# Kernel optimization log

Hardware: AMD Instinct MI355X
Metric: run time of the kernel (lower is better)

The kernel has to match this reference:

```python
import math
import jax, jax.numpy as jnp
import numpy as np

L = 2          # num_layers
B = 2          # micro batch
S = 2048       # seq_length
H = 1024       # hidden_size
NH = 16        # num_attention_heads
DH = 64        # kv_channels (head dim)
FF = 4096      # ffn_hidden_size
EPS = 1e-5
STD = 0.0048


def setup_inputs() -> dict:
    key = jax.random.key(0)
    ks = jax.random.split(key, 12)
    out_std = STD / math.sqrt(2.0 * L)
    # ALiBi slopes for NH=16 (power of 2)
    start = 2.0 ** (-2.0 ** (-(math.log2(NH) - 3)))
    slopes = np.array([start * start ** i for i in range(NH)], dtype=np.float32)
    alibi = slopes[None, :, None, None] * np.arange(S, dtype=np.float32)[None, None, None, :]
    alibi = jnp.asarray(np.broadcast_to(alibi, (B, NH, 1, S)))  # [B, NH, 1, S]
    return {
        "hidden_states": jax.random.normal(ks[0], (B, S, H), jnp.float32),
        "alibi": alibi,
        "qkv_w": jax.random.normal(ks[1], (L, 3 * NH * DH, H), jnp.float32) * STD,
        "qkv_b": jnp.zeros((L, 3 * NH * DH), jnp.float32),
        "dense_w": jax.random.normal(ks[2], (L, H, NH * DH), jnp.float32) * out_std,
        "dense_b": jnp.zeros((L, H), jnp.float32),
        "mlp_w1": jax.random.normal(ks[3], (L, FF, H), jnp.float32) * STD,
        "mlp_b1": jnp.zeros((L, FF), jnp.float32),
        "mlp_w2": jax.random.normal(ks[4], (L, H, FF), jnp.float32) * out_std,
        "mlp_b2": jnp.zeros((L, H), jnp.float32),
        "ln1_w": jnp.ones((L, H), jnp.float32),
        "ln1_b": jnp.zeros((L, H), jnp.float32),
        "ln2_w": jnp.ones((L, H), jnp.float32),
        "ln2_b": jnp.zeros((L, H), jnp.float32),
    }


def _layernorm(x, w, b):
    mu = jnp.mean(x, axis=-1, keepdims=True)
    var = jnp.mean(jnp.square(x - mu), axis=-1, keepdims=True)
    return (x - mu) * jax.lax.rsqrt(var + EPS) * w + b


def _layer(x, alibi, causal, layer_number, qkv_w, qkv_b, dense_w, dense_b,
           mlp_w1, mlp_b1, mlp_w2, mlp_b2, ln1_w, ln1_b, ln2_w, ln2_b):
    # --- attention ---
    h = _layernorm(x, ln1_w, ln1_b)
    qkv = h @ qkv_w.T + qkv_b                       # [B, S, 3*NH*DH]
    q, k, v = jnp.split(qkv, 3, axis=-1)
    q = q.reshape(B, S, NH, DH).transpose(0, 2, 1, 3)  # [B, NH, S, DH]
    k = k.reshape(B, S, NH, DH).transpose(0, 2, 1, 3)
    v = v.reshape(B, S, NH, DH).transpose(0, 2, 1, 3)
    norm_factor = math.sqrt(DH) * layer_number
    beta = 1.0 / layer_number
    alpha = 1.0 / norm_factor
    scores = beta * alibi + alpha * jnp.einsum("bhqd,bhkd->bhqk", q, k)
    # ScaleMaskSoftmax: scale by layer_number, causal mask fill -10000, softmax
    scores = scores * layer_number
    scores = jnp.where(causal, scores, jnp.float32(-10000.0))
    probs = jax.nn.softmax(scores, axis=-1)
    ctx = jnp.einsum("bhqk,bhkd->bhqd", probs, v)   # [B, NH, S, DH]
    ctx = ctx.transpose(0, 2, 1, 3).reshape(B, S, NH * DH)
    attn_out = ctx @ dense_w.T + dense_b
    x = x + attn_out
    # --- MLP ---
    h2 = _layernorm(x, ln2_w, ln2_b)
    m = jax.nn.gelu(h2 @ mlp_w1.T + mlp_b1, approximate=False)
    m = m @ mlp_w2.T + mlp_b2
    return x + m


def reference(hidden_states, alibi, qkv_w, qkv_b, dense_w, dense_b,
              mlp_w1, mlp_b1, mlp_w2, mlp_b2, ln1_w, ln1_b, ln2_w, ln2_b):
    causal = jnp.tril(jnp.ones((S, S), dtype=bool))[None, None]  # [1,1,S,S]
    x = hidden_states
    for l in range(L):
        x = _layer(x, alibi, causal, l + 1,
                   qkv_w[l], qkv_b[l], dense_w[l], dense_b[l],
                   mlp_w1[l], mlp_b1[l], mlp_w2[l], mlp_b2[l],
                   ln1_w[l], ln1_b[l], ln2_w[l], ln2_b[l])
    return x
```

## Files before the change

kernel.cpp:

```cpp
#include <hip/hip_runtime.h>
#include <cstdint>
#include <cmath>

#define SS 2048
#define HH 1024

typedef __bf16 bf16_t;
typedef __bf16 bf16x8 __attribute__((ext_vector_type(8)));
typedef __bf16 bf16x4 __attribute__((ext_vector_type(4)));
typedef float  f32x4  __attribute__((ext_vector_type(4)));

union U32P { unsigned u; bf16_t h[2]; };

__device__ __forceinline__ void async_load16(const void* g, void* l) {
  __builtin_amdgcn_global_load_lds(
      (__attribute__((address_space(1))) void*)(g),
      (__attribute__((address_space(3))) void*)(l), 16, 0, 0);
}

__global__ __launch_bounds__(256) void cvt_kernel(const float* __restrict__ in,
                                                  bf16_t* __restrict__ out) {
  size_t i = (size_t)blockIdx.x * 256 + threadIdx.x;
  f32x4 v = ((const f32x4*)in)[i];
  bf16x4 o;
  o[0] = (bf16_t)v[0]; o[1] = (bf16_t)v[1]; o[2] = (bf16_t)v[2]; o[3] = (bf16_t)v[3];
  ((bf16x4*)out)[i] = o;
}

__global__ __launch_bounds__(256) void ln_kernel(const float* __restrict__ x,
                                                 const float* __restrict__ w,
                                                 const float* __restrict__ b,
                                                 bf16_t* __restrict__ out) {
  const int row = blockIdx.x;
  const int tid = threadIdx.x;
  const f32x4 v = ((const f32x4*)(x + (size_t)row * HH))[tid];
  float s  = v[0] + v[1] + v[2] + v[3];
  float s2 = v[0]*v[0] + v[1]*v[1] + v[2]*v[2] + v[3]*v[3];
#pragma unroll
  for (int o = 1; o < 64; o <<= 1) { s += __shfl_xor(s, o); s2 += __shfl_xor(s2, o); }
  __shared__ float r1[4], r2[4];
  if ((tid & 63) == 0) { r1[tid >> 6] = s; r2[tid >> 6] = s2; }
  __syncthreads();
  float ts  = r1[0] + r1[1] + r1[2] + r1[3];
  float ts2 = r2[0] + r2[1] + r2[2] + r2[3];
  float mu  = ts * (1.0f / HH);
  float var = ts2 * (1.0f / HH) - mu * mu;
  float rstd = rsqrtf(var + 1e-5f);
  f32x4 wv = ((const f32x4*)w)[tid];
  f32x4 bv = ((const f32x4*)b)[tid];
  bf16x4 o;
#pragma unroll
  for (int j = 0; j < 4; ++j) o[j] = (bf16_t)((v[j] - mu) * rstd * wv[j] + bv[j]);
  ((bf16x4*)(out + (size_t)row * HH))[tid] = o;
}

__device__ __forceinline__ float gelu_f(float x) {
  return 0.5f * x * (1.0f + erff(x * 0.70710678118654752f));
}

__global__ __launch_bounds__(256) void fuse_add(float* __restrict__ x,
                                                const bf16_t* __restrict__ p0,
                                                const bf16_t* __restrict__ p1,
                                                const float* __restrict__ bias) {
  size_t i = (size_t)blockIdx.x * 256 + threadIdx.x;
  f32x4 xv = ((f32x4*)x)[i];
  bf16x4 a = ((const bf16x4*)p0)[i];
  bf16x4 b4 = ((const bf16x4*)p1)[i];
  f32x4 bv = ((const f32x4*)bias)[i & 255];
#pragma unroll
  for (int j = 0; j < 4; ++j) xv[j] += (float)a[j] + (float)b4[j] + bv[j];
  ((f32x4*)x)[i] = xv;
}

template <int EPI>
__global__ __launch_bounds__(256) void gemm_bt(const bf16_t* __restrict__ A,
                                               const bf16_t* __restrict__ W,
                                               const float* __restrict__ bias,
                                               bf16_t* __restrict__ outb,
                                               int M, int N, int K) {
  __shared__ __align__(16) bf16_t As[128 * 64];
  __shared__ __align__(16) bf16_t Bs[128 * 64];
  const int tid = threadIdx.x;
  const int w = tid >> 6, lane = tid & 63;
  const int m16 = lane & 15, quad = lane >> 4;
  const int wm = w & 1, wn = w >> 1;
  const int n0 = blockIdx.x * 128, m0 = blockIdx.y * 128;

  f32x4 acc[4][4];
#pragma unroll
  for (int i = 0; i < 4; ++i)
#pragma unroll
    for (int j = 0; j < 4; ++j) acc[i][j] = (f32x4){0.f, 0.f, 0.f, 0.f};

  int rowi[4], gci[4];
#pragma unroll
  for (int i = 0; i < 4; ++i) {
    int p = (w * 4 + i) * 64 + lane;
    rowi[i] = p >> 3;
    gci[i] = ((lane & 7) ^ (rowi[i] & 7)) * 8;
  }

  for (int kt = 0; kt < K; kt += 64) {
    __syncthreads();
#pragma unroll
    for (int i = 0; i < 4; ++i) {
      async_load16(A + (size_t)(m0 + rowi[i]) * K + kt + gci[i], &As[(w * 4 + i) * 512]);
      async_load16(W + (size_t)(n0 + rowi[i]) * K + kt + gci[i], &Bs[(w * 4 + i) * 512]);
    }
    __syncthreads();
#pragma unroll
    for (int kk = 0; kk < 2; ++kk) {
      bf16x8 af[4], bfv[4];
#pragma unroll
      for (int mi = 0; mi < 4; ++mi) {
        int row = wm * 64 + mi * 16 + m16;
        int cpos = (kk * 4 + quad) ^ (row & 7);
        af[mi] = *(const bf16x8*)&As[row * 64 + cpos * 8];
      }
#pragma unroll
      for (int ni = 0; ni < 4; ++ni) {
        int row = wn * 64 + ni * 16 + m16;
        int cpos = (kk * 4 + quad) ^ (row & 7);
        bfv[ni] = *(const bf16x8*)&Bs[row * 64 + cpos * 8];
      }
#pragma unroll
      for (int mi = 0; mi < 4; ++mi)
#pragma unroll
        for (int ni = 0; ni < 4; ++ni)
          acc[mi][ni] = __builtin_amdgcn_mfma_f32_16x16x32_bf16(af[mi], bfv[ni],
                                                                acc[mi][ni], 0, 0, 0);
    }
  }

#pragma unroll
  for (int ni = 0; ni < 4; ++ni) {
    int col = n0 + wn * 64 + ni * 16 + m16;
    float bv = bias[col];
#pragma unroll
    for (int mi = 0; mi < 4; ++mi) {
      int rowb = m0 + wm * 64 + mi * 16 + quad * 4;
#pragma unroll
      for (int r = 0; r < 4; ++r) {
        size_t idx = (size_t)(rowb + r) * N + col;
        float v = acc[mi][ni][r] + bv;
        if constexpr (EPI == 1) v = gelu_f(v);
        outb[idx] = (bf16_t)v;
      }
    }
  }
}

__global__ __launch_bounds__(256) void gemm_sk2(const bf16_t* __restrict__ A,
                                                const bf16_t* __restrict__ W,
                                                bf16_t* __restrict__ p0,
                                                bf16_t* __restrict__ p1,
                                                int M, int N, int K) {
  __shared__ __align__(16) bf16_t As[128 * 64];
  __shared__ __align__(16) bf16_t Bs[128 * 64];
  const int tid = threadIdx.x;
  const int w = tid >> 6, lane = tid & 63;
  const int m16 = lane & 15, quad = lane >> 4;
  const int wm = w & 1, wn = w >> 1;
  const int n0 = blockIdx.x * 128, m0 = blockIdx.y * 128;
  const int z = blockIdx.z;
  const int kbeg = z * (K >> 1), kend = kbeg + (K >> 1);
  bf16_t* outb = z ? p1 : p0;

  f32x4 acc[4][4];
#pragma unroll
  for (int i = 0; i < 4; ++i)
#pragma unroll
    for (int j = 0; j < 4; ++j) acc[i][j] = (f32x4){0.f, 0.f, 0.f, 0.f};

  int rowi[4], gci[4];
#pragma unroll
  for (int i = 0; i < 4; ++i) {
    int p = (w * 4 + i) * 64 + lane;
    rowi[i] = p >> 3;
    gci[i] = ((lane & 7) ^ (rowi[i] & 7)) * 8;
  }

  for (int kt = kbeg; kt < kend; kt += 64) {
    __syncthreads();
#pragma unroll
    for (int i = 0; i < 4; ++i) {
      async_load16(A + (size_t)(m0 + rowi[i]) * K + kt + gci[i], &As[(w * 4 + i) * 512]);
      async_load16(W + (size_t)(n0 + rowi[i]) * K + kt + gci[i], &Bs[(w * 4 + i) * 512]);
    }
    __syncthreads();
#pragma unroll
    for (int kk = 0; kk < 2; ++kk) {
      bf16x8 af[4], bfv[4];
#pragma unroll
      for (int mi = 0; mi < 4; ++mi) {
        int row = wm * 64 + mi * 16 + m16;
        int cpos = (kk * 4 + quad) ^ (row & 7);
        af[mi] = *(const bf16x8*)&As[row * 64 + cpos * 8];
      }
#pragma unroll
      for (int ni = 0; ni < 4; ++ni) {
        int row = wn * 64 + ni * 16 + m16;
        int cpos = (kk * 4 + quad) ^ (row & 7);
        bfv[ni] = *(const bf16x8*)&Bs[row * 64 + cpos * 8];
      }
#pragma unroll
      for (int mi = 0; mi < 4; ++mi)
#pragma unroll
        for (int ni = 0; ni < 4; ++ni)
          acc[mi][ni] = __builtin_amdgcn_mfma_f32_16x16x32_bf16(af[mi], bfv[ni],
                                                                acc[mi][ni], 0, 0, 0);
    }
  }

#pragma unroll
  for (int ni = 0; ni < 4; ++ni) {
    int col = n0 + wn * 64 + ni * 16 + m16;
#pragma unroll
    for (int mi = 0; mi < 4; ++mi) {
      int rowb = m0 + wm * 64 + mi * 16 + quad * 4;
#pragma unroll
      for (int r = 0; r < 4; ++r) {
        size_t idx = (size_t)(rowb + r) * N + col;
        outb[idx] = (bf16_t)acc[mi][ni][r];
      }
    }
  }
}

__global__ __launch_bounds__(256) void attn_kernel(const bf16_t* __restrict__ qkv,
                                                   bf16_t* __restrict__ ctx) {
  const int qt = 31 - blockIdx.y;
  const int bh = blockIdx.x;
  const int b = bh >> 4, h = bh & 15;
  const int tid = threadIdx.x;
  const int w = tid >> 6, lane = tid & 63;
  const int m16 = lane & 15, quad = lane >> 4;

  __shared__ __align__(16) bf16_t Vt[2][64 * 72];
  __shared__ __align__(16) bf16_t Pl[4][16 * 72];

  const float slope2 = __builtin_amdgcn_exp2f(-0.70710678118654752f * (float)(h + 1))
                       * 1.4426950408889634f;
  const int wt = (int)((30.0f / slope2 + 63.0f) * 0.015625f);
  const int kt0 = (qt - wt > 0) ? (qt - wt) : 0;

  const int q_abs = qt * 64 + w * 16 + m16;
  float alkb[16];
#pragma unroll
  for (int kn = 0; kn < 4; ++kn)
#pragma unroll
    for (int r = 0; r < 4; ++r)
      alkb[kn * 4 + r] = slope2 * (float)(kt0 * 64 + kn * 16 + quad * 4 + r - q_abs);
  const float d64 = slope2 * 64.0f;

  const int qrow = qt * 64 + w * 16 + m16;
  const bf16_t* qbase = qkv + (size_t)(b * SS + qrow) * 3072 + h * 64;
  const bf16x8 bq0 = *(const bf16x8*)(qbase + quad * 8);
  const bf16x8 bq1 = *(const bf16x8*)(qbase + 32 + quad * 8);

  const bf16_t* kbase = qkv + (size_t)(b * SS + m16) * 3072 + 1024 + h * 64 + quad * 8;
  const int kp2 = (tid & 31) * 2, vd0 = (tid >> 5) * 8;
  const bf16_t* vsrc = qkv + (size_t)(b * SS + kp2) * 3072 + 2048 + h * 64 + vd0;
  const int ql = w * 16 + m16;
  constexpr float C = 0.18033688011112042f;

  f32x4 acc[4];
#pragma unroll
  for (int i = 0; i < 4; ++i) acc[i] = (f32x4){0.f, 0.f, 0.f, 0.f};
  float rs_l = 0.f;

  bf16x8 ak[4][2], v0, v1;
  {
    const bf16_t* kb = kbase + (size_t)kt0 * 64 * 3072;
#pragma unroll
    for (int kn = 0; kn < 4; ++kn) {
      ak[kn][0] = *(const bf16x8*)(kb + (size_t)(kn * 16) * 3072);
      ak[kn][1] = *(const bf16x8*)(kb + (size_t)(kn * 16) * 3072 + 32);
    }
    const bf16_t* vs = vsrc + (size_t)kt0 * 64 * 3072;
    v0 = *(const bf16x8*)(vs);
    v1 = *(const bf16x8*)(vs + 3072);
  }
#pragma unroll
  for (int j = 0; j < 8; ++j) {
    U32P pk; pk.h[0] = v0[j]; pk.h[1] = v1[j];
    *(unsigned*)&Vt[kt0 & 1][(vd0 + j) * 72 + kp2] = pk.u;
  }

  for (int kt = kt0; kt <= qt; ++kt) {
    __syncthreads();

    bf16x8 nk[4][2], nv0 = v0, nv1 = v1;
    if (kt < qt) {
      const bf16_t* kb = kbase + (size_t)(kt + 1) * 64 * 3072;
#pragma unroll
      for (int kn = 0; kn < 4; ++kn) {
        nk[kn][0] = *(const bf16x8*)(kb + (size_t)(kn * 16) * 3072);
        nk[kn][1] = *(const bf16x8*)(kb + (size_t)(kn * 16) * 3072 + 32);
      }
      const bf16_t* nsrc = vsrc + (size_t)(kt + 1) * 64 * 3072;
      nv0 = *(const bf16x8*)(nsrc);
      nv1 = *(const bf16x8*)(nsrc + 3072);
    } else {
#pragma unroll
      for (int kn = 0; kn < 4; ++kn) { nk[kn][0] = ak[kn][0]; nk[kn][1] = ak[kn][1]; }
    }

    float p[16];
    const bool diag = (kt == qt);
#pragma unroll
    for (int kn = 0; kn < 4; ++kn) {
      f32x4 z = (f32x4){0.f, 0.f, 0.f, 0.f};
      z = __builtin_amdgcn_mfma_f32_16x16x32_bf16(ak[kn][0], bq0, z, 0, 0, 0);
      z = __builtin_amdgcn_mfma_f32_16x16x32_bf16(ak[kn][1], bq1, z, 0, 0, 0);
#pragma unroll
      for (int r = 0; r < 4; ++r) {
        float s = fmaf(z[r], C, alkb[kn * 4 + r]);
        if (diag) {
          int kl = kn * 16 + quad * 4 + r;
          if (kl > ql) s = -INFINITY;
        }
        float e = __builtin_amdgcn_exp2f(s);
        p[kn * 4 + r] = e;
        rs_l += e;
      }
    }
#pragma unroll
    for (int i = 0; i < 16; ++i) alkb[i] += d64;

#pragma unroll
    for (int kn = 0; kn < 4; ++kn) {
      U32P a, c;
      a.h[0] = (bf16_t)p[kn * 4 + 0]; a.h[1] = (bf16_t)p[kn * 4 + 1];
      c.h[0] = (bf16_t)p[kn * 4 + 2]; c.h[1] = (bf16_t)p[kn * 4 + 3];
      uint2 pk; pk.x = a.u; pk.y = c.u;
      *(uint2*)&Pl[w][m16 * 72 + kn * 16 + quad * 4] = pk;
    }
    const bf16_t* vt = &Vt[kt & 1][0];
    bf16x8 bp0 = *(const bf16x8*)&Pl[w][m16 * 72 + quad * 8];
    bf16x8 bp1 = *(const bf16x8*)&Pl[w][m16 * 72 + 32 + quad * 8];
#pragma unroll
    for (int ni = 0; ni < 4; ++ni) {
      bf16x8 av0 = *(const bf16x8*)&vt[(ni * 16 + m16) * 72 + quad * 8];
      bf16x8 av1 = *(const bf16x8*)&vt[(ni * 16 + m16) * 72 + 32 + quad * 8];
      acc[ni] = __builtin_amdgcn_mfma_f32_16x16x32_bf16(av0, bp0, acc[ni], 0, 0, 0);
      acc[ni] = __builtin_amdgcn_mfma_f32_16x16x32_bf16(av1, bp1, acc[ni], 0, 0, 0);
    }

    if (kt < qt) {
#pragma unroll
      for (int j = 0; j < 8; ++j) {
        U32P pk; pk.h[0] = nv0[j]; pk.h[1] = nv1[j];
        *(unsigned*)&Vt[(kt + 1) & 1][(vd0 + j) * 72 + kp2] = pk.u;
      }
    }
#pragma unroll
    for (int kn = 0; kn < 4; ++kn) { ak[kn][0] = nk[kn][0]; ak[kn][1] = nk[kn][1]; }
    v0 = nv0; v1 = nv1;
  }

  rs_l += __shfl_xor(rs_l, 16);
  rs_l += __shfl_xor(rs_l, 32);
  const float inv_l = 1.0f / rs_l;
  bf16_t* cb = ctx + (size_t)(b * SS + qt * 64 + w * 16 + m16) * 1024 + h * 64;
#pragma unroll
  for (int ni = 0; ni < 4; ++ni) {
    U32P a, c;
    a.h[0] = (bf16_t)(acc[ni][0] * inv_l); a.h[1] = (bf16_t)(acc[ni][1] * inv_l);
    c.h[0] = (bf16_t)(acc[ni][2] * inv_l); c.h[1] = (bf16_t)(acc[ni][3] * inv_l);
    uint2 pk; pk.x = a.u; pk.y = c.u;
    *(uint2*)(cb + ni * 16 + quad * 4) = pk;
  }
}

extern "C" void kernel_launch(void* const* d_in, const int* in_sizes, int n_in,
                              void* d_out, int out_size, void* d_ws, size_t ws_size,
                              hipStream_t stream) {
  const float* hs    = (const float*)d_in[0];
  const float* qkvw  = (const float*)d_in[2];
  const float* qkvb  = (const float*)d_in[3];
  const float* dw    = (const float*)d_in[4];
  const float* db    = (const float*)d_in[5];
  const float* w1    = (const float*)d_in[6];
  const float* b1    = (const float*)d_in[7];
  const float* w2    = (const float*)d_in[8];
  const float* b2    = (const float*)d_in[9];
  const float* ln1w  = (const float*)d_in[10];
  const float* ln1b  = (const float*)d_in[11];
  const float* ln2w  = (const float*)d_in[12];
  const float* ln2b  = (const float*)d_in[13];
  float* x = (float*)d_out;

  char* ws = (char*)d_ws;
  bf16_t* wqc = (bf16_t*)(ws + 0);
  bf16_t* wdc = (bf16_t*)(ws + 12582912);
  bf16_t* w1c = (bf16_t*)(ws + 16777216);
  bf16_t* w2c = (bf16_t*)(ws + 33554432);
  bf16_t* hb  = (bf16_t*)(ws + 50331648);
  bf16_t* qm  = (bf16_t*)(ws + 58720256);
  bf16_t* cx  = (bf16_t*)(ws + 92274688);
  bf16_t* dp0 = qm;
  bf16_t* dp1 = qm + (size_t)4096 * 1024;

  hipMemcpyAsync(x, hs, (size_t)4096 * 1024 * 4, hipMemcpyDeviceToDevice, stream);
  cvt_kernel<<<6144, 256, 0, stream>>>(qkvw, wqc);
  cvt_kernel<<<2048, 256, 0, stream>>>(dw, wdc);
  cvt_kernel<<<8192, 256, 0, stream>>>(w1, w1c);
  cvt_kernel<<<8192, 256, 0, stream>>>(w2, w2c);

  for (int l = 0; l < 2; ++l) {
    ln_kernel<<<4096, 256, 0, stream>>>(x, ln1w + l * 1024, ln1b + l * 1024, hb);
    gemm_bt<0><<<dim3(24, 32), 256, 0, stream>>>(hb, wqc + (size_t)l * 3145728,
        qkvb + l * 3072, qm, 4096, 3072, 1024);
    attn_kernel<<<dim3(32, 32), 256, 0, stream>>>(qm, cx);
    gemm_sk2<<<dim3(8, 32, 2), 256, 0, stream>>>(cx, wdc + (size_t)l * 1048576,
        dp0, dp1, 4096, 1024, 1024);
    fuse_add<<<4096, 256, 0, stream>>>(x, dp0, dp1, db + l * 1024);
    ln_kernel<<<4096, 256, 0, stream>>>(x, ln2w + l * 1024, ln2b + l * 1024, hb);
    gemm_bt<1><<<dim3(32, 32), 256, 0, stream>>>(hb, w1c + (size_t)l * 4194304,
        b1 + l * 4096, qm, 4096, 4096, 1024);
    gemm_sk2<<<dim3(8, 32, 2), 256, 0, stream>>>(qm, w2c + (size_t)l * 4194304,
        hb, cx, 4096, 1024, 4096);
    fuse_add<<<4096, 256, 0, stream>>>(x, hb, cx, b2 + l * 1024);
  }
}
```

Before: 706.8 us.

## Emit per-head Q/K and transposed V from QKV GEMM; one-wave LDS-free attention

The QKV GEMM epilogue now writes Q row-major, K in a per-(batch, head) contiguous layout and V transposed per head. This lets the attention kernel load MFMA operands straight from global memory. Attention is rewritten so each wave independently handles 16 query rows, stepping 32 keys at a time with no shared memory or block barriers. The ALiBi slope constant now matches the reference slopes, which also changes the truncated key window. Weight conversion to bf16 moves into the per-layer loop to shrink the workspace. The trade-off is scattered, strided epilogue stores for K and V, and more global-load traffic per wave.

```diff
diff --git a/kernel.cpp b/kernel.cpp
--- a/kernel.cpp
+++ b/kernel.cpp
@@ -145,6 +145,99 @@
         float v = acc[mi][ni][r] + bv;
         if constexpr (EPI == 1) v = gelu_f(v);
         outb[idx] = (bf16_t)v;
+      }
+    }
+  }
+}
+
+__global__ __launch_bounds__(256) void gemm_qkv(const bf16_t* __restrict__ A,
+                                                const bf16_t* __restrict__ W,
+                                                const float* __restrict__ bias,
+                                                bf16_t* __restrict__ qq,
+                                                bf16_t* __restrict__ kpb,
+                                                bf16_t* __restrict__ vtb) {
+  __shared__ __align__(16) bf16_t As[128 * 64];
+  __shared__ __align__(16) bf16_t Bs[128 * 64];
+  const int K = 1024;
+  const int tid = threadIdx.x;
+  const int w = tid >> 6, lane = tid & 63;
+  const int m16 = lane & 15, quad = lane >> 4;
+  const int wm = w & 1, wn = w >> 1;
+  const int n0 = blockIdx.x * 128, m0 = blockIdx.y * 128;
+
+  f32x4 acc[4][4];
+#pragma unroll
+  for (int i = 0; i < 4; ++i)
+#pragma unroll
+    for (int j = 0; j < 4; ++j) acc[i][j] = (f32x4){0.f, 0.f, 0.f, 0.f};
+
+  int rowi[4], gci[4];
+#pragma unroll
+  for (int i = 0; i < 4; ++i) {
+    int p = (w * 4 + i) * 64 + lane;
+    rowi[i] = p >> 3;
+    gci[i] = ((lane & 7) ^ (rowi[i] & 7)) * 8;
+  }
+
+  for (int kt = 0; kt < K; kt += 64) {
+    __syncthreads();
+#pragma unroll
+    for (int i = 0; i < 4; ++i) {
+      async_load16(A + (size_t)(m0 + rowi[i]) * K + kt + gci[i], &As[(w * 4 + i) * 512]);
+      async_load16(W + (size_t)(n0 + rowi[i]) * K + kt + gci[i], &Bs[(w * 4 + i) * 512]);
+    }
+    __syncthreads();
+#pragma unroll
+    for (int kk = 0; kk < 2; ++kk) {
+      bf16x8 af[4], bfv[4];
+#pragma unroll
+      for (int mi = 0; mi < 4; ++mi) {
+        int row = wm * 64 + mi * 16 + m16;
+        int cpos = (kk * 4 + quad) ^ (row & 7);
+        af[mi] = *(const bf16x8*)&As[row * 64 + cpos * 8];
+      }
+#pragma unroll
+      for (int ni = 0; ni < 4; ++ni) {
+        int row = wn * 64 + ni * 16 + m16;
+        int cpos = (kk * 4 + quad) ^ (row & 7);
+        bfv[ni] = *(const bf16x8*)&Bs[row * 64 + cpos * 8];
+      }
+#pragma unroll
+      for (int mi = 0; mi < 4; ++mi)
+#pragma unroll
+        for (int ni = 0; ni < 4; ++ni)
+          acc[mi][ni] = __builtin_amdgcn_mfma_f32_16x16x32_bf16(af[mi], bfv[ni],
+                                                                acc[mi][ni], 0, 0, 0);
+    }
+  }
+
+  const int sec = n0 >> 10;
+#pragma unroll
+  for (int ni = 0; ni < 4; ++ni) {
+    int col = n0 + wn * 64 + ni * 16 + m16;
+    float bv = bias[col];
+    int c2 = col & 1023, hh = c2 >> 6, d = c2 & 63;
+#pragma unroll
+    for (int mi = 0; mi < 4; ++mi) {
+      int rowb = m0 + wm * 64 + mi * 16 + quad * 4;
+      int bb = rowb >> 11, t = rowb & 2047;
+      float v[4];
+#pragma unroll
+      for (int r = 0; r < 4; ++r) v[r] = acc[mi][ni][r] + bv;
+      if (sec == 0) {
+#pragma unroll
+        for (int r = 0; r < 4; ++r)
+          qq[(size_t)(rowb + r) * 1024 + col] = (bf16_t)v[r];
+      } else if (sec == 1) {
+        bf16_t* kdst = kpb + (((size_t)(bb * 16 + hh) * 2048 + t) * 64 + d);
+#pragma unroll
+        for (int r = 0; r < 4; ++r) kdst[r * 64] = (bf16_t)v[r];
+      } else {
+        U32P a2, c3;
+        a2.h[0] = (bf16_t)v[0]; a2.h[1] = (bf16_t)v[1];
+        c3.h[0] = (bf16_t)v[2]; c3.h[1] = (bf16_t)v[3];
+        uint2 pk; pk.x = a2.u; pk.y = c3.u;
+        *(uint2*)(vtb + (((size_t)(bb * 16 + hh) * 64 + d) * 2048 + t)) = pk;
       }
     }
   }
@@ -227,149 +320,109 @@
   }
 }
 
-__global__ __launch_bounds__(256) void attn_kernel(const bf16_t* __restrict__ qkv,
-                                                   bf16_t* __restrict__ ctx) {
-  const int qt = 31 - blockIdx.y;
-  const int bh = blockIdx.x;
+__global__ __launch_bounds__(256, 4) void attn_kernel(const bf16_t* __restrict__ qq,
+                                                      const bf16_t* __restrict__ kp,
+                                                      const bf16_t* __restrict__ vT,
+                                                      bf16_t* __restrict__ ctx) {
+  const int u = blockIdx.x * 4 + (threadIdx.x >> 6);
+  const int bh = u & 31;
+  const int q16 = 127 - (u >> 5);
   const int b = bh >> 4, h = bh & 15;
-  const int tid = threadIdx.x;
-  const int w = tid >> 6, lane = tid & 63;
+  const int lane = threadIdx.x & 63;
   const int m16 = lane & 15, quad = lane >> 4;
-
-  __shared__ __align__(16) bf16_t Vt[2][64 * 72];
-  __shared__ __align__(16) bf16_t Pl[4][16 * 72];
-
-  const float slope2 = __builtin_amdgcn_exp2f(-0.70710678118654752f * (float)(h + 1))
+  const int q_lo = q16 << 4, q_hi = q_lo + 15;
+
+  const float slope2 = __builtin_amdgcn_exp2f(-0.5f * (float)(h + 1))
                        * 1.4426950408889634f;
-  const int wt = (int)((30.0f / slope2 + 63.0f) * 0.015625f);
-  const int kt0 = (qt - wt > 0) ? (qt - wt) : 0;
-
-  const int q_abs = qt * 64 + w * 16 + m16;
-  float alkb[16];
-#pragma unroll
-  for (int kn = 0; kn < 4; ++kn)
-#pragma unroll
-    for (int r = 0; r < 4; ++r)
-      alkb[kn * 4 + r] = slope2 * (float)(kt0 * 64 + kn * 16 + quad * 4 + r - q_abs);
-  const float d64 = slope2 * 64.0f;
-
-  const int qrow = qt * 64 + w * 16 + m16;
-  const bf16_t* qbase = qkv + (size_t)(b * SS + qrow) * 3072 + h * 64;
-  const bf16x8 bq0 = *(const bf16x8*)(qbase + quad * 8);
-  const bf16x8 bq1 = *(const bf16x8*)(qbase + 32 + quad * 8);
-
-  const bf16_t* kbase = qkv + (size_t)(b * SS + m16) * 3072 + 1024 + h * 64 + quad * 8;
-  const int kp2 = (tid & 31) * 2, vd0 = (tid >> 5) * 8;
-  const bf16_t* vsrc = qkv + (size_t)(b * SS + kp2) * 3072 + 2048 + h * 64 + vd0;
-  const int ql = w * 16 + m16;
+  int k_min = q_lo - (int)(30.0f / slope2);
+  k_min = (k_min < 0) ? 0 : (k_min & ~31);
+
+  const bf16_t* qb = qq + (size_t)(b * SS + q_lo + m16) * 1024 + h * 64 + quad * 8;
+  const bf16x8 bq0 = *(const bf16x8*)(qb);
+  const bf16x8 bq1 = *(const bf16x8*)(qb + 32);
+
+  const int rX = ((m16 >> 2) << 3) + (m16 & 3);
+  const bf16_t* kb0 = kp + ((size_t)bh * 2048 + rX) * 64 + quad * 8;
+  const bf16_t* vb0 = vT + ((size_t)bh * 64 + m16) * 2048 + quad * 8;
+
+  const float d32 = slope2 * 32.0f;
+  float alkX[4], alkY[4];
+#pragma unroll
+  for (int r = 0; r < 4; ++r) {
+    alkX[r] = slope2 * (float)(k_min + quad * 8 + r - q_lo - m16);
+    alkY[r] = alkX[r] + slope2 * 4.0f;
+  }
+
+  f32x4 acc[4];
+#pragma unroll
+  for (int i = 0; i < 4; ++i) acc[i] = (f32x4){0.f, 0.f, 0.f, 0.f};
+  float rs = 0.f;
   constexpr float C = 0.18033688011112042f;
 
-  f32x4 acc[4];
-#pragma unroll
-  for (int i = 0; i < 4; ++i) acc[i] = (f32x4){0.f, 0.f, 0.f, 0.f};
-  float rs_l = 0.f;
-
-  bf16x8 ak[4][2], v0, v1;
+  bf16x8 aX0, aX1, aY0, aY1;
   {
-    const bf16_t* kb = kbase + (size_t)kt0 * 64 * 3072;
-#pragma unroll
-    for (int kn = 0; kn < 4; ++kn) {
-      ak[kn][0] = *(const bf16x8*)(kb + (size_t)(kn * 16) * 3072);
-      ak[kn][1] = *(const bf16x8*)(kb + (size_t)(kn * 16) * 3072 + 32);
-    }
-    const bf16_t* vs = vsrc + (size_t)kt0 * 64 * 3072;
-    v0 = *(const bf16x8*)(vs);
-    v1 = *(const bf16x8*)(vs + 3072);
-  }
-#pragma unroll
-  for (int j = 0; j < 8; ++j) {
-    U32P pk; pk.h[0] = v0[j]; pk.h[1] = v1[j];
-    *(unsigned*)&Vt[kt0 & 1][(vd0 + j) * 72 + kp2] = pk.u;
-  }
-
-  for (int kt = kt0; kt <= qt; ++kt) {
-    __syncthreads();
-
-    bf16x8 nk[4][2], nv0 = v0, nv1 = v1;
-    if (kt < qt) {
-      const bf16_t* kb = kbase + (size_t)(kt + 1) * 64 * 3072;
-#pragma unroll
-      for (int kn = 0; kn < 4; ++kn) {
-        nk[kn][0] = *(const bf16x8*)(kb + (size_t)(kn * 16) * 3072);
-        nk[kn][1] = *(const bf16x8*)(kb + (size_t)(kn * 16) * 3072 + 32);
-      }
-      const bf16_t* nsrc = vsrc + (size_t)(kt + 1) * 64 * 3072;
-      nv0 = *(const bf16x8*)(nsrc);
-      nv1 = *(const bf16x8*)(nsrc + 3072);
-    } else {
-#pragma unroll
-      for (int kn = 0; kn < 4; ++kn) { nk[kn][0] = ak[kn][0]; nk[kn][1] = ak[kn][1]; }
-    }
-
-    float p[16];
-    const bool diag = (kt == qt);
-#pragma unroll
-    for (int kn = 0; kn < 4; ++kn) {
-      f32x4 z = (f32x4){0.f, 0.f, 0.f, 0.f};
-      z = __builtin_amdgcn_mfma_f32_16x16x32_bf16(ak[kn][0], bq0, z, 0, 0, 0);
-      z = __builtin_amdgcn_mfma_f32_16x16x32_bf16(ak[kn][1], bq1, z, 0, 0, 0);
-#pragma unroll
-      for (int r = 0; r < 4; ++r) {
-        float s = fmaf(z[r], C, alkb[kn * 4 + r]);
-        if (diag) {
-          int kl = kn * 16 + quad * 4 + r;
-          if (kl > ql) s = -INFINITY;
-        }
-        float e = __builtin_amdgcn_exp2f(s);
-        p[kn * 4 + r] = e;
-        rs_l += e;
-      }
-    }
-#pragma unroll
-    for (int i = 0; i < 16; ++i) alkb[i] += d64;
-
-#pragma unroll
-    for (int kn = 0; kn < 4; ++kn) {
-      U32P a, c;
-      a.h[0] = (bf16_t)p[kn * 4 + 0]; a.h[1] = (bf16_t)p[kn * 4 + 1];
-      c.h[0] = (bf16_t)p[kn * 4 + 2]; c.h[1] = (bf16_t)p[kn * 4 + 3];
-      uint2 pk; pk.x = a.u; pk.y = c.u;
-      *(uint2*)&Pl[w][m16 * 72 + kn * 16 + quad * 4] = pk;
-    }
-    const bf16_t* vt = &Vt[kt & 1][0];
-    bf16x8 bp0 = *(const bf16x8*)&Pl[w][m16 * 72 + quad * 8];
-    bf16x8 bp1 = *(const bf16x8*)&Pl[w][m16 * 72 + 32 + quad * 8];
-#pragma unroll
-    for (int ni = 0; ni < 4; ++ni) {
-      bf16x8 av0 = *(const bf16x8*)&vt[(ni * 16 + m16) * 72 + quad * 8];
-      bf16x8 av1 = *(const bf16x8*)&vt[(ni * 16 + m16) * 72 + 32 + quad * 8];
-      acc[ni] = __builtin_amdgcn_mfma_f32_16x16x32_bf16(av0, bp0, acc[ni], 0, 0, 0);
-      acc[ni] = __builtin_amdgcn_mfma_f32_16x16x32_bf16(av1, bp1, acc[ni], 0, 0, 0);
-    }
-
-    if (kt < qt) {
-#pragma unroll
-      for (int j = 0; j < 8; ++j) {
-        U32P pk; pk.h[0] = nv0[j]; pk.h[1] = nv1[j];
-        *(unsigned*)&Vt[(kt + 1) & 1][(vd0 + j) * 72 + kp2] = pk.u;
-      }
-    }
-#pragma unroll
-    for (int kn = 0; kn < 4; ++kn) { ak[kn][0] = nk[kn][0]; ak[kn][1] = nk[kn][1]; }
-    v0 = nv0; v1 = nv1;
-  }
-
-  rs_l += __shfl_xor(rs_l, 16);
-  rs_l += __shfl_xor(rs_l, 32);
-  const float inv_l = 1.0f / rs_l;
-  bf16_t* cb = ctx + (size_t)(b * SS + qt * 64 + w * 16 + m16) * 1024 + h * 64;
-#pragma unroll
-  for (int ni = 0; ni < 4; ++ni) {
-    U32P a, c;
-    a.h[0] = (bf16_t)(acc[ni][0] * inv_l); a.h[1] = (bf16_t)(acc[ni][1] * inv_l);
-    c.h[0] = (bf16_t)(acc[ni][2] * inv_l); c.h[1] = (bf16_t)(acc[ni][3] * inv_l);
-    uint2 pk; pk.x = a.u; pk.y = c.u;
-    *(uint2*)(cb + ni * 16 + quad * 4) = pk;
+    const bf16_t* kx = kb0 + (size_t)k_min * 64;
+    aX0 = *(const bf16x8*)(kx);
+    aX1 = *(const bf16x8*)(kx + 32);
+    aY0 = *(const bf16x8*)(kx + 256);
+    aY1 = *(const bf16x8*)(kx + 288);
+  }
+
+  for (int kb = k_min; kb <= q_hi; kb += 32) {
+    const bf16_t* vx = vb0 + kb;
+    bf16x8 av0 = *(const bf16x8*)(vx);
+    bf16x8 av1 = *(const bf16x8*)(vx + 16 * 2048);
+    bf16x8 av2 = *(const bf16x8*)(vx + 32 * 2048);
+    bf16x8 av3 = *(const bf16x8*)(vx + 48 * 2048);
+    bf16x8 nX0 = aX0, nX1 = aX1, nY0 = aY0, nY1 = aY1;
+    if (kb + 32 <= q_hi) {
+      const bf16_t* kx = kb0 + (size_t)(kb + 32) * 64;
+      nX0 = *(const bf16x8*)(kx);
+      nX1 = *(const bf16x8*)(kx + 32);
+      nY0 = *(const bf16x8*)(kx + 256);
+      nY1 = *(const bf16x8*)(kx + 288);
+    }
+
+    f32x4 zX = (f32x4){0.f, 0.f, 0.f, 0.f};
+    zX = __builtin_amdgcn_mfma_f32_16x16x32_bf16(aX0, bq0, zX, 0, 0, 0);
+    zX = __builtin_amdgcn_mfma_f32_16x16x32_bf16(aX1, bq1, zX, 0, 0, 0);
+    f32x4 zY = (f32x4){0.f, 0.f, 0.f, 0.f};
+    zY = __builtin_amdgcn_mfma_f32_16x16x32_bf16(aY0, bq0, zY, 0, 0, 0);
+    zY = __builtin_amdgcn_mfma_f32_16x16x32_bf16(aY1, bq1, zY, 0, 0, 0);
+
+    bf16x8 bp;
+#pragma unroll
+    for (int r = 0; r < 4; ++r) {
+      float sX = fmaf(zX[r], C, alkX[r]);
+      float sY = fmaf(zY[r], C, alkY[r]);
+      float eX = (alkX[r] > 0.0f) ? 0.0f : __builtin_amdgcn_exp2f(sX);
+      float eY = (alkY[r] > 0.0f) ? 0.0f : __builtin_amdgcn_exp2f(sY);
+      bp[r] = (bf16_t)eX;
+      bp[4 + r] = (bf16_t)eY;
+      rs += eX + eY;
+      alkX[r] += d32;
+      alkY[r] += d32;
+    }
+
+    acc[0] = __builtin_amdgcn_mfma_f32_16x16x32_bf16(av0, bp, acc[0], 0, 0, 0);
+    acc[1] = __builtin_amdgcn_mfma_f32_16x16x32_bf16(av1, bp, acc[1], 0, 0, 0);
+    acc[2] = __builtin_amdgcn_mfma_f32_16x16x32_bf16(av2, bp, acc[2], 0, 0, 0);
+    acc[3] = __builtin_amdgcn_mfma_f32_16x16x32_bf16(av3, bp, acc[3], 0, 0, 0);
+
+    aX0 = nX0; aX1 = nX1; aY0 = nY0; aY1 = nY1;
+  }
+
+  rs += __shfl_xor(rs, 16);
+  rs += __shfl_xor(rs, 32);
+  const float inv = 1.0f / rs;
+  bf16_t* cb = ctx + (size_t)(b * SS + q_lo + m16) * 1024 + h * 64 + quad * 4;
+#pragma unroll
+  for (int s = 0; s < 4; ++s) {
+    U32P a2, c2;
+    a2.h[0] = (bf16_t)(acc[s][0] * inv); a2.h[1] = (bf16_t)(acc[s][1] * inv);
+    c2.h[0] = (bf16_t)(acc[s][2] * inv); c2.h[1] = (bf16_t)(acc[s][3] * inv);
+    uint2 pk; pk.x = a2.u; pk.y = c2.u;
+    *(uint2*)(cb + s * 16) = pk;
   }
 }
 
@@ -392,35 +445,37 @@
   float* x = (float*)d_out;
 
   char* ws = (char*)d_ws;
-  bf16_t* wqc = (bf16_t*)(ws + 0);
-  bf16_t* wdc = (bf16_t*)(ws + 12582912);
-  bf16_t* w1c = (bf16_t*)(ws + 16777216);
-  bf16_t* w2c = (bf16_t*)(ws + 33554432);
-  bf16_t* hb  = (bf16_t*)(ws + 50331648);
-  bf16_t* qm  = (bf16_t*)(ws + 58720256);
-  bf16_t* cx  = (bf16_t*)(ws + 92274688);
-  bf16_t* dp0 = qm;
-  bf16_t* dp1 = qm + (size_t)4096 * 1024;
+  bf16_t* wq  = (bf16_t*)(ws + 0);
+  bf16_t* wd  = (bf16_t*)(ws + 6291456);
+  bf16_t* w1c = (bf16_t*)(ws + 8388608);
+  bf16_t* w2c = (bf16_t*)(ws + 16777216);
+  bf16_t* hb  = (bf16_t*)(ws + 25165824);
+  bf16_t* qq  = (bf16_t*)(ws + 33554432);
+  bf16_t* kpb = (bf16_t*)(ws + 41943040);
+  bf16_t* vtb = (bf16_t*)(ws + 50331648);
+  bf16_t* cx  = (bf16_t*)(ws + 58720256);
+  bf16_t* qmid = (bf16_t*)(ws + 33554432);
+  bf16_t* p2b = (bf16_t*)(ws + 67108864);
+  bf16_t* dp0 = qq;
+  bf16_t* dp1 = kpb;
 
   hipMemcpyAsync(x, hs, (size_t)4096 * 1024 * 4, hipMemcpyDeviceToDevice, stream);
-  cvt_kernel<<<6144, 256, 0, stream>>>(qkvw, wqc);
-  cvt_kernel<<<2048, 256, 0, stream>>>(dw, wdc);
-  cvt_kernel<<<8192, 256, 0, stream>>>(w1, w1c);
-  cvt_kernel<<<8192, 256, 0, stream>>>(w2, w2c);
 
   for (int l = 0; l < 2; ++l) {
+    cvt_kernel<<<3072, 256, 0, stream>>>(qkvw + (size_t)l * 3145728, wq);
+    cvt_kernel<<<1024, 256, 0, stream>>>(dw + (size_t)l * 1048576, wd);
+    cvt_kernel<<<4096, 256, 0, stream>>>(w1 + (size_t)l * 4194304, w1c);
+    cvt_kernel<<<4096, 256, 0, stream>>>(w2 + (size_t)l * 4194304, w2c);
+
     ln_kernel<<<4096, 256, 0, stream>>>(x, ln1w + l * 1024, ln1b + l * 1024, hb);
-    gemm_bt<0><<<dim3(24, 32), 256, 0, stream>>>(hb, wqc + (size_t)l * 3145728,
-        qkvb + l * 3072, qm, 4096, 3072, 1024);
-    attn_kernel<<<dim3(32, 32), 256, 0, stream>>>(qm, cx);
-    gemm_sk2<<<dim3(8, 32, 2), 256, 0, stream>>>(cx, wdc + (size_t)l * 1048576,
-        dp0, dp1, 4096, 1024, 1024);
+    gemm_qkv<<<dim3(24, 32), 256, 0, stream>>>(hb, wq, qkvb + l * 3072, qq, kpb, vtb);
+    attn_kernel<<<1024, 256, 0, stream>>>(qq, kpb, vtb, cx);
+    gemm_sk2<<<dim3(8, 32, 2), 256, 0, stream>>>(cx, wd, dp0, dp1, 4096, 1024, 1024);
     fuse_add<<<4096, 256, 0, stream>>>(x, dp0, dp1, db + l * 1024);
     ln_kernel<<<4096, 256, 0, stream>>>(x, ln2w + l * 1024, ln2b + l * 1024, hb);
-    gemm_bt<1><<<dim3(32, 32), 256, 0, stream>>>(hb, w1c + (size_t)l * 4194304,
-        b1 + l * 4096, qm, 4096, 4096, 1024);
-    gemm_sk2<<<dim3(8, 32, 2), 256, 0, stream>>>(qm, w2c + (size_t)l * 4194304,
-        hb, cx, 4096, 1024, 4096);
-    fuse_add<<<4096, 256, 0, stream>>>(x, hb, cx, b2 + l * 1024);
-  }
-}
+    gemm_bt<1><<<dim3(32, 32), 256, 0, stream>>>(hb, w1c, b1 + l * 4096, qmid,
+                                                 4096, 4096, 1024);
+    gemm_sk2<<<dim3(8, 32, 2), 256, 0, stream>>>(qmid, w2c, hb, p2b, 4096, 1024, 4096);
+    fuse_add<<<4096, 256, 0, stream>>>(x, hb, p2b, b2 + l * 1024);
+  }
+}
```

Result: slower. 843.8 us (+19.4%).
